# Optimization experiments

Hardware: AMD Instinct MI355X
Metric: run time of the kernel (lower is better)

## Reference

```python
import jax, jax.numpy as jnp
import numpy as np

B, L, H, P = 4, 8192, 256, 256


def discretize(log_real, imag, log_Delta, B_real, B_imag):
    # Lambda = -exp(log_real) + i*imag ; ZOH discretization
    Lr = -jnp.exp(log_real)
    Li = imag
    Delta = jnp.exp(log_Delta)
    ad = Lr * Delta
    bd = Li * Delta
    exp_ad = jnp.exp(ad)
    Lbar_r = exp_ad * jnp.cos(bd)
    Lbar_i = exp_ad * jnp.sin(bd)
    denom = jnp.maximum(Lr * Lr + Li * Li, 1e-12)
    inv_Lr = Lr / denom
    inv_Li = -Li / denom
    diff_r = Lbar_r - 1.0
    diff_i = Lbar_i
    coeff_r = inv_Lr * diff_r - inv_Li * diff_i
    coeff_i = inv_Lr * diff_i + inv_Li * diff_r
    B_bar_r = coeff_r[:, None] * B_real - coeff_i[:, None] * B_imag
    B_bar_i = coeff_r[:, None] * B_imag + coeff_i[:, None] * B_real
    return Lbar_r, Lbar_i, B_bar_r, B_bar_i


def binop(ei, ej):
    Ar_i, Ai_i, xr_i, xi_i = ei
    Ar_j, Ai_j, xr_j, xi_j = ej
    return (Ar_j * Ar_i - Ai_j * Ai_i,
            Ar_j * Ai_i + Ai_j * Ar_i,
            Ar_j * xr_i - Ai_j * xi_i + xr_j,
            Ar_j * xi_i + Ai_j * xr_i + xi_j)


def apply_ssm(Lbar_r, Lbar_i, B_bar_r, B_bar_i, C_real, C_imag, D, x):
    # x: (B,L,H), B_bar: (P,H), C: (H,P)
    Bu_r = jnp.einsum('blh,ph->blp', x, B_bar_r)
    Bu_i = jnp.einsum('blh,ph->blp', x, B_bar_i)
    A_r = jnp.broadcast_to(Lbar_r, Bu_r.shape)
    A_i = jnp.broadcast_to(Lbar_i, Bu_i.shape)
    _, _, xs_r, xs_i = jax.lax.associative_scan(binop, (A_r, A_i, Bu_r, Bu_i), axis=1)
    ys = jnp.einsum('blp,hp->blh', xs_r, C_real) - jnp.einsum('blp,hp->blh', xs_i, C_imag)
    return ys + D * x


def s5(log_real, imag, log_Delta, B_real, B_imag, C_real, C_imag, D, x):
    Lbar_r, Lbar_i, B_bar_r, B_bar_i = discretize(log_real, imag, log_Delta, B_real, B_imag)
    y = apply_ssm(Lbar_r, Lbar_i, B_bar_r, B_bar_i, C_real, C_imag, D, x)
    return jax.nn.gelu(y, approximate=False)


def setup_inputs() -> dict:
    key = jax.random.key(0)
    ks = jax.random.split(key, 17)
    std_b = 1.0 / H ** 0.5
    std_c = 1.0 / P ** 0.5
    def params(ki):
        k = jax.random.split(ks[ki], 8)
        return dict(
            log_real=jax.random.normal(k[0], (P,), jnp.float32) * 0.5,
            imag=jax.random.normal(k[1], (P,), jnp.float32),
            log_Delta=jnp.zeros((P,), jnp.float32),
            B_real=jax.random.normal(k[2], (P, H), jnp.float32) * std_b,
            B_imag=jax.random.normal(k[3], (P, H), jnp.float32) * std_b,
            C_real=jax.random.normal(k[4], (H, P), jnp.float32) * std_c,
            C_imag=jax.random.normal(k[5], (H, P), jnp.float32) * std_c,
            D=jnp.ones((H,), jnp.float32),
        )
    f = params(1)
    b = params(2)
    inp = {'x': jax.random.normal(ks[0], (B, L, H), jnp.float32)}
    for name, v in f.items():
        inp['fwd_' + name] = v
    for name, v in b.items():
        inp['bwd_' + name] = v
    return inp


def reference(x,
              fwd_log_real, fwd_imag, fwd_log_Delta, fwd_B_real, fwd_B_imag,
              fwd_C_real, fwd_C_imag, fwd_D,
              bwd_log_real, bwd_imag, bwd_log_Delta, bwd_B_real, bwd_B_imag,
              bwd_C_real, bwd_C_imag, bwd_D):
    x_flip = jnp.flip(x, axis=1)
    y_f = s5(fwd_log_real, fwd_imag, fwd_log_Delta, fwd_B_real, fwd_B_imag,
             fwd_C_real, fwd_C_imag, fwd_D, x)
    y_b = s5(bwd_log_real, bwd_imag, bwd_log_Delta, bwd_B_real, bwd_B_imag,
             bwd_C_real, bwd_C_imag, bwd_D, x_flip)
    return y_f + jnp.flip(y_b, axis=1)
```

## Files before the change

### kernel.cpp

```cpp
#include <hip/hip_runtime.h>
#include <math.h>

#define B_DIM 4
#define L_DIM 8192
#define H_DIM 256
#define P_DIM 256
#define M_DIM (B_DIM * L_DIM)
#define NC 64
#define LC 128

typedef __attribute__((ext_vector_type(8))) short bf16x8;
typedef __attribute__((ext_vector_type(4))) float f32x4;

static __device__ __forceinline__ float bf2f(unsigned int u) {
    union { unsigned int i; float f; } v; v.i = u << 16; return v.f;
}
static __device__ __forceinline__ unsigned short f2bf(float f) {
    union { float f; unsigned int i; } v; v.f = f;
    unsigned int r = v.i + 0x7FFFu + ((v.i >> 16) & 1u);
    return (unsigned short)(r >> 16);
}
static __device__ __forceinline__ float gelu_f(float x) {
    float z = 0.7978845608028654f * (x + 0.044715f * x * x * x);
    float e = __expf(2.0f * z);
    float t = 1.0f - 2.0f / (e + 1.0f);
    return 0.5f * x * (1.0f + t);
}
static __device__ __forceinline__ void async_load16(const void* g, void* l) {
    __builtin_amdgcn_global_load_lds(
        (const __attribute__((address_space(1))) unsigned int*)g,
        (__attribute__((address_space(3))) unsigned int*)l, 16, 0, 0);
}

__global__ void prep_kernel(const float* fLr, const float* fIm, const float* fLd,
                            const float* fBr, const float* fBi,
                            const float* fCr, const float* fCi,
                            const float* bLr, const float* bIm, const float* bLd,
                            const float* bBr, const float* bBi,
                            const float* bCr, const float* bCi,
                            const float4* __restrict__ x4, ushort4* __restrict__ xb,
                            unsigned short* Bmat, unsigned short* B3, float2* LbarWS) {
    int gid = blockIdx.x * 256 + threadIdx.x;
    if (gid < 2097152) {
        float4 v = x4[gid];
        ushort4 o;
        o.x = f2bf(v.x); o.y = f2bf(v.y); o.z = f2bf(v.z); o.w = f2bf(v.w);
        xb[gid] = o;
        return;
    }
    int g1 = gid - 2097152;
    if (g1 < 262144) {
        int k = g1 >> 8, h = g1 & 255;
        int d = k >> 9, pc = k & 511, p = pc >> 1, comp = pc & 1;
        const float* LR = d ? bLr : fLr;
        const float* IM = d ? bIm : fIm;
        const float* LD = d ? bLd : fLd;
        const float* BR = d ? bBr : fBr;
        const float* BI = d ? bBi : fBi;
        float Lr = -expf(LR[p]);
        float Li = IM[p];
        float Delta = expf(LD[p]);
        float ea = expf(Lr * Delta);
        float bd = Li * Delta;
        float Lbr = ea * cosf(bd);
        float Lbi = ea * sinf(bd);
        float denom = fmaxf(Lr * Lr + Li * Li, 1e-12f);
        float ivr = Lr / denom, ivi = -Li / denom;
        float dr = Lbr - 1.0f, di = Lbi;
        float cr = ivr * dr - ivi * di;
        float ci = ivr * di + ivi * dr;
        float br = BR[p * 256 + h], bi = BI[p * 256 + h];
        float val = comp ? (cr * bi + ci * br) : (cr * br - ci * bi);
        Bmat[g1] = f2bf(val);
    } else if (g1 < 524288) {
        int g2 = g1 - 262144;
        int d = g2 >> 17;
        int rem = g2 & 131071;
        int h = rem >> 9;
        int kk = rem & 511;
        int p = kk >> 1, comp = kk & 1;
        const float* CR = d ? bCr : fCr;
        const float* CI = d ? bCi : fCi;
        float val = comp ? -CI[h * 256 + p] : CR[h * 256 + p];
        B3[g2] = f2bf(val);
    } else if (g1 < 524800) {
        int g2 = g1 - 524288;
        int d = g2 >> 8, p = g2 & 255;
        const float* LR = d ? bLr : fLr;
        const float* IM = d ? bIm : fIm;
        const float* LD = d ? bLd : fLd;
        float Lr = -expf(LR[p]); float Li = IM[p]; float Delta = expf(LD[p]);
        float ea = expf(Lr * Delta); float bd = Li * Delta;
        LbarWS[g2] = make_float2(ea * cosf(bd), ea * sinf(bd));
    }
}

__global__ __launch_bounds__(256, 2) void k1_gemm(const unsigned short* __restrict__ A,
                                                  const unsigned short* __restrict__ Bm,
                                                  unsigned short* __restrict__ Bu,
                                                  const float2* __restrict__ Lbar,
                                                  float2* __restrict__ carry,
                                                  float2* __restrict__ halfc) {
    __shared__ unsigned short SH[16384];
    __shared__ float2 Sbuf[64];
    int tid = threadIdx.x;
    int lane = tid & 63, wv = tid >> 6;
    int wm = (wv >> 1) * 64, wn = (wv & 1) * 64;
    int Mb = blockIdx.x * 128, Nb = blockIdx.y * 128;
    int lr = lane >> 3;
    int swz = ((lane & 7) ^ lr) * 8;
    f32x4 acc[4][4];
#pragma unroll
    for (int i = 0; i < 4; i++)
#pragma unroll
        for (int j = 0; j < 4; j++) acc[i][j] = (f32x4){0.f, 0.f, 0.f, 0.f};
    int mrow = lane & 15, quad = lane >> 4;
    for (int kb = 0; kb < 256; kb += 64) {
#pragma unroll
        for (int ch = wv; ch < 16; ch += 4) {
            int r = ch * 8 + lr;
            async_load16(A  + (size_t)(Mb + r) * 256 + kb + swz, (char*)SH + ch * 1024);
            async_load16(Bm + (size_t)(Nb + r) * 256 + kb + swz, (char*)SH + 16384 + ch * 1024);
        }
        __syncthreads();
#pragma unroll
        for (int kk = 0; kk < 64; kk += 32) {
            bf16x8 af[4], bfr[4];
#pragma unroll
            for (int i = 0; i < 4; i++) {
                int rr = wm + 16 * i + mrow;
                af[i] = *(const bf16x8*)&SH[rr * 64 + ((((kk >> 3) + quad) ^ (rr & 7)) << 3)];
            }
#pragma unroll
            for (int j = 0; j < 4; j++) {
                int rr = wn + 16 * j + mrow;
                bfr[j] = *(const bf16x8*)&SH[8192 + rr * 64 + ((((kk >> 3) + quad) ^ (rr & 7)) << 3)];
            }
#pragma unroll
            for (int i = 0; i < 4; i++)
#pragma unroll
                for (int j = 0; j < 4; j++)
                    acc[i][j] = __builtin_amdgcn_mfma_f32_16x16x32_bf16(af[i], bfr[j], acc[i][j], 0, 0, 0);
        }
        __syncthreads();
    }
    unsigned short* Cs = SH;
#pragma unroll
    for (int i = 0; i < 4; i++)
#pragma unroll
        for (int j = 0; j < 4; j++)
#pragma unroll
            for (int r = 0; r < 4; r++) {
                int row = wm + 16 * i + quad * 4 + r;
                int col = wn + 16 * j + mrow;
                Cs[row * 128 + col] = f2bf(acc[i][j][r]);
            }
    __syncthreads();
#pragma unroll
    for (int it = 0; it < 8; it++) {
        int o = tid * 16 + it * 4096;
        int row = o >> 8, colb = o & 255;
        uint4 v = *(const uint4*)((const char*)Cs + o);
        *(uint4*)((char*)Bu + (size_t)(Mb + row) * 2048 + (size_t)Nb * 2 + colb) = v;
    }
    int d = Nb >> 9;
    int b = Mb >> 13;
    int c = (Mb >> 7) & 63;
    float sr = 0.f, si = 0.f;
    float2 A2 = make_float2(0.f, 0.f);
    int p = 0;
    if (tid < 128) {
        int j = tid & 63, half = tid >> 6;
        p = ((Nb & 511) >> 1) + j;
        A2 = Lbar[d * 256 + p];
        const unsigned int* C32 = (const unsigned int*)Cs;
        int r0 = half * 64;
        if (d == 0) {
            for (int t = 0; t < 64; t++) {
                unsigned int v = C32[(r0 + t) * 64 + j];
                float zr = bf2f(v & 0xffffu), zi = bf2f(v >> 16);
                float nr = A2.x * sr - A2.y * si + zr;
                float ni = A2.x * si + A2.y * sr + zi;
                sr = nr; si = ni;
            }
        } else {
            for (int t = 63; t >= 0; t--) {
                unsigned int v = C32[(r0 + t) * 64 + j];
                float zr = bf2f(v & 0xffffu), zi = bf2f(v >> 16);
                float nr = A2.x * sr - A2.y * si + zr;
                float ni = A2.x * si + A2.y * sr + zi;
                sr = nr; si = ni;
            }
        }
        if (half == 1) Sbuf[j] = make_float2(sr, si);
    }
    __syncthreads();
    if (tid < 64) {
        float2 S1 = Sbuf[tid];
        float a64r = A2.x, a64i = A2.y;
#pragma unroll
        for (int k = 0; k < 6; k++) {
            float nr = a64r * a64r - a64i * a64i;
            float ni = 2.f * a64r * a64i;
            a64r = nr; a64i = ni;
        }
        float cr, ci;
        float2 hv;
        if (d == 0) {
            cr = a64r * sr - a64i * si + S1.x;
            ci = a64r * si + a64i * sr + S1.y;
            hv = make_float2(sr, si);
        } else {
            cr = sr + a64r * S1.x - a64i * S1.y;
            ci = si + a64r * S1.y + a64i * S1.x;
            hv = S1;
        }
        size_t cidx = ((size_t)(d * 4 + b) * NC + c) * 256 + p;
        carry[cidx] = make_float2(cr, ci);
        halfc[cidx] = hv;
    }
}

__global__ __launch_bounds__(512) void scan_fix_kernel(unsigned int* __restrict__ XSu,
                                                       const float2* __restrict__ Lbar,
                                                       const float2* __restrict__ carry,
                                                       const float2* __restrict__ halfc) {
    int m = blockIdx.x, b = blockIdx.y;
    int c = m >> 1, h = m & 1;
    int d = threadIdx.x >> 8;
    int p = threadIdx.x & 255;
    float2 A = Lbar[d * 256 + p];
    float ar = A.x, ai = A.y;
    float a64r = ar, a64i = ai;
#pragma unroll
    for (int k = 0; k < 6; k++) {
        float nr = a64r * a64r - a64i * a64i;
        float ni = 2.f * a64r * a64i;
        a64r = nr; a64i = ni;
    }
    float a128r = a64r * a64r - a64i * a64i;
    float a128i = 2.f * a64r * a64i;
    float sr = 0.f, si = 0.f;
    const float2* cb = carry + ((size_t)(d * 4 + b) * NC) * 256 + p;
    size_t hidx = ((size_t)(d * 4 + b) * NC + c) * 256 + p;
    if (d == 0) {
#pragma unroll 4
        for (int j = 0; j < c; j++) {
            float2 cj = cb[(size_t)j * 256];
            float nr = a128r * sr - a128i * si + cj.x;
            float ni = a128r * si + a128i * sr + cj.y;
            sr = nr; si = ni;
        }
        if (h) {
            float2 hc = halfc[hidx];
            float nr = a64r * sr - a64i * si + hc.x;
            float ni = a64r * si + a64i * sr + hc.y;
            sr = nr; si = ni;
        }
    } else {
#pragma unroll 4
        for (int j = NC - 1; j > c; j--) {
            float2 cj = cb[(size_t)j * 256];
            float nr = a128r * sr - a128i * si + cj.x;
            float ni = a128r * si + a128i * sr + cj.y;
            sr = nr; si = ni;
        }
        if (!h) {
            float2 hc = halfc[hidx];
            float nr = a64r * sr - a64i * si + hc.x;
            float ni = a64r * si + a64i * sr + hc.y;
            sr = nr; si = ni;
        }
    }
    size_t base = (size_t)b * L_DIM * 512 + d * 256 + p;
    int l0 = c * 128 + h * 64;
    if (d == 0) {
#pragma unroll 16
        for (int t = 0; t < 64; t++) {
            size_t idx = base + (size_t)(l0 + t) * 512;
            unsigned int v = XSu[idx];
            float zr = bf2f(v & 0xffffu), zi = bf2f(v >> 16);
            float nr = ar * sr - ai * si + zr;
            float ni = ar * si + ai * sr + zi;
            sr = nr; si = ni;
            XSu[idx] = (unsigned int)f2bf(sr) | ((unsigned int)f2bf(si) << 16);
        }
    } else {
#pragma unroll 16
        for (int t = 63; t >= 0; t--) {
            size_t idx = base + (size_t)(l0 + t) * 512;
            unsigned int v = XSu[idx];
            float zr = bf2f(v & 0xffffu), zi = bf2f(v >> 16);
            float nr = ar * sr - ai * si + zr;
            float ni = ar * si + ai * sr + zi;
            sr = nr; si = ni;
            XSu[idx] = (unsigned int)f2bf(sr) | ((unsigned int)f2bf(si) << 16);
        }
    }
}

static __device__ __forceinline__ void k3_half(const unsigned short* __restrict__ XS,
                                               const unsigned short* __restrict__ B3h,
                                               unsigned short* As, unsigned short* Bs,
                                               int Mb, int Hb, int coff,
                                               int wm, int wn, int mrow, int quad,
                                               int lr, int swz, int wv,
                                               f32x4 (&acc)[4][4]) {
    for (int kb = 0; kb < 512; kb += 64) {
#pragma unroll
        for (int ch = wv; ch < 16; ch += 4) {
            int r = ch * 8 + lr;
            async_load16(XS + (size_t)(Mb + r) * 1024 + coff + kb + swz, (char*)As + ch * 1024);
            async_load16(B3h + (size_t)(Hb + r) * 512 + kb + swz, (char*)Bs + ch * 1024);
        }
        __syncthreads();
#pragma unroll
        for (int kk = 0; kk < 64; kk += 32) {
            bf16x8 af[4], bfr[4];
#pragma unroll
            for (int i = 0; i < 4; i++) {
                int rr = wm + 16 * i + mrow;
                af[i] = *(const bf16x8*)&As[rr * 64 + ((((kk >> 3) + quad) ^ (rr & 7)) << 3)];
            }
#pragma unroll
            for (int j = 0; j < 4; j++) {
                int rr = wn + 16 * j + mrow;
                bfr[j] = *(const bf16x8*)&Bs[rr * 64 + ((((kk >> 3) + quad) ^ (rr & 7)) << 3)];
            }
#pragma unroll
            for (int i = 0; i < 4; i++)
#pragma unroll
                for (int j = 0; j < 4; j++)
                    acc[i][j] = __builtin_amdgcn_mfma_f32_16x16x32_bf16(af[i], bfr[j], acc[i][j], 0, 0, 0);
        }
        __syncthreads();
    }
}

__global__ __launch_bounds__(256, 2) void k3_gemm(const unsigned short* __restrict__ XS,
                                                  const unsigned short* __restrict__ B3,
                                                  const unsigned short* __restrict__ xbf,
                                                  const float* __restrict__ Df,
                                                  const float* __restrict__ Db,
                                                  float* __restrict__ out) {
    __shared__ unsigned short As[128 * 64];
    __shared__ unsigned short Bs[128 * 64];
    int tid = threadIdx.x;
    int lane = tid & 63, wv = tid >> 6;
    int wm = (wv >> 1) * 64, wn = (wv & 1) * 64;
    int Mb = blockIdx.x * 128, Hb = blockIdx.y * 128;
    int lr = lane >> 3;
    int swz = ((lane & 7) ^ lr) * 8;
    int mrow = lane & 15, quad = lane >> 4;
    f32x4 accf[4][4], accb[4][4];
#pragma unroll
    for (int i = 0; i < 4; i++)
#pragma unroll
        for (int j = 0; j < 4; j++) {
            accf[i][j] = (f32x4){0.f, 0.f, 0.f, 0.f};
            accb[i][j] = (f32x4){0.f, 0.f, 0.f, 0.f};
        }
    k3_half(XS, B3,          As, Bs, Mb, Hb, 0,   wm, wn, mrow, quad, lr, swz, wv, accf);
    k3_half(XS, B3 + 131072, As, Bs, Mb, Hb, 512, wm, wn, mrow, quad, lr, swz, wv, accb);
#pragma unroll
    for (int i = 0; i < 4; i++)
#pragma unroll
        for (int j = 0; j < 4; j++) {
            int h = Hb + wn + 16 * j + mrow;
            float df = Df[h], db = Db[h];
#pragma unroll
            for (int r = 0; r < 4; r++) {
                int row = Mb + wm + 16 * i + quad * 4 + r;
                float xv = bf2f((unsigned int)xbf[(size_t)row * 256 + h]);
                float yf = accf[i][j][r] + df * xv;
                float yb = accb[i][j][r] + db * xv;
                out[(size_t)row * 256 + h] = gelu_f(yf) + gelu_f(yb);
            }
        }
}

extern "C" void kernel_launch(void* const* d_in, const int* in_sizes, int n_in,
                              void* d_out, int out_size, void* d_ws, size_t ws_size,
                              hipStream_t stream) {
    const float* x   = (const float*)d_in[0];
    const float* fLr = (const float*)d_in[1];
    const float* fIm = (const float*)d_in[2];
    const float* fLd = (const float*)d_in[3];
    const float* fBr = (const float*)d_in[4];
    const float* fBi = (const float*)d_in[5];
    const float* fCr = (const float*)d_in[6];
    const float* fCi = (const float*)d_in[7];
    const float* fD  = (const float*)d_in[8];
    const float* bLr = (const float*)d_in[9];
    const float* bIm = (const float*)d_in[10];
    const float* bLd = (const float*)d_in[11];
    const float* bBr = (const float*)d_in[12];
    const float* bBi = (const float*)d_in[13];
    const float* bCr = (const float*)d_in[14];
    const float* bCi = (const float*)d_in[15];
    const float* bD  = (const float*)d_in[16];
    float* out = (float*)d_out;

    char* ws = (char*)d_ws;
    unsigned short* xbf  = (unsigned short*)(ws);
    unsigned short* Bu   = (unsigned short*)(ws + 16777216);
    unsigned short* Bmat = (unsigned short*)(ws + 16777216 + 67108864);
    unsigned short* B3   = (unsigned short*)(ws + 16777216 + 67108864 + 524288);
    float2* LbarWS = (float2*)(ws + 16777216 + 67108864 + 1048576);
    float2* carry  = (float2*)(ws + 16777216 + 67108864 + 1048576 + 4096);
    float2* halfc  = (float2*)(ws + 16777216 + 67108864 + 1048576 + 4096 + 1048576);

    prep_kernel<<<10242, 256, 0, stream>>>(fLr, fIm, fLd, fBr, fBi, fCr, fCi,
                                           bLr, bIm, bLd, bBr, bBi, bCr, bCi,
                                           (const float4*)x, (ushort4*)xbf,
                                           Bmat, B3, LbarWS);
    k1_gemm<<<dim3(256, 8), 256, 0, stream>>>(xbf, Bmat, Bu, LbarWS, carry, halfc);
    scan_fix_kernel<<<dim3(128, 4), 512, 0, stream>>>((unsigned int*)Bu, LbarWS, carry, halfc);
    k3_gemm<<<dim3(256, 2), 256, 0, stream>>>(Bu, B3, xbf, fD, bD, out);
}
```

Before: 199.4 us.

## Fuse chunk scan fix-up into output GEMM using per-16-row carry snapshots

Removes the separate scan_fix kernel, which re-read and rewrote the whole Bu buffer. k1 now records the scan state at every 16 rows and writes 8 sub-chunk prefixes per chunk. k3 first combines the chunk carries into a prefix, then rescans each 16-row slice of the A tile in shared memory before the MFMA step. This saves a full read-modify-write pass over the 64MB intermediate. In exchange it adds serial scan work, an extra barrier per k-step and redundant carry prefix loops inside the GEMM kernel, and its UL, Ptab and LbarL arrays add about 24KB of shared memory per block.

Result: no change. 199.4 us (-0.0%).

```diff
diff --git a/kernel.cpp b/kernel.cpp
--- a/kernel.cpp
+++ b/kernel.cpp
@@ -30,6 +30,15 @@
     __builtin_amdgcn_global_load_lds(
         (const __attribute__((address_space(1))) unsigned int*)g,
         (__attribute__((address_space(3))) unsigned int*)l, 16, 0, 0);
+}
+static __device__ __forceinline__ float2 cmul2(float2 a, float2 b) {
+    return make_float2(a.x * b.x - a.y * b.y, a.x * b.y + a.y * b.x);
+}
+static __device__ __forceinline__ float2 csq2(float2 a) {
+    return make_float2(a.x * a.x - a.y * a.y, 2.f * a.x * a.y);
+}
+static __device__ __forceinline__ float2 cmad(float2 A, float2 s, float2 z) {
+    return make_float2(A.x * s.x - A.y * s.y + z.x, A.x * s.y + A.y * s.x + z.y);
 }
 
 __global__ void prep_kernel(const float* fLr, const float* fIm, const float* fLd,
@@ -100,9 +109,9 @@
                                                   unsigned short* __restrict__ Bu,
                                                   const float2* __restrict__ Lbar,
                                                   float2* __restrict__ carry,
-                                                  float2* __restrict__ halfc) {
+                                                  float2* __restrict__ Usub) {
     __shared__ unsigned short SH[16384];
-    __shared__ float2 Sbuf[64];
+    __shared__ float2 Sbuf2[64][4];
     int tid = threadIdx.x;
     int lane = tid & 63, wv = tid >> 6;
     int wm = (wv >> 1) * 64, wn = (wv & 1) * 64;
@@ -166,8 +175,10 @@
     int d = Nb >> 9;
     int b = Mb >> 13;
     int c = (Mb >> 7) & 63;
-    float sr = 0.f, si = 0.f;
+    float2 s = make_float2(0.f, 0.f);
     float2 A2 = make_float2(0.f, 0.f);
+    float2 snap[3];
+    snap[0] = snap[1] = snap[2] = make_float2(0.f, 0.f);
     int p = 0;
     if (tid < 128) {
         int j = tid & 63, half = tid >> 6;
@@ -178,134 +189,77 @@
         if (d == 0) {
             for (int t = 0; t < 64; t++) {
                 unsigned int v = C32[(r0 + t) * 64 + j];
-                float zr = bf2f(v & 0xffffu), zi = bf2f(v >> 16);
-                float nr = A2.x * sr - A2.y * si + zr;
-                float ni = A2.x * si + A2.y * sr + zi;
-                sr = nr; si = ni;
+                float2 z = make_float2(bf2f(v & 0xffffu), bf2f(v >> 16));
+                s = cmad(A2, s, z);
+                if ((t & 15) == 15 && t < 63) snap[t >> 4] = s;
             }
         } else {
             for (int t = 63; t >= 0; t--) {
                 unsigned int v = C32[(r0 + t) * 64 + j];
-                float zr = bf2f(v & 0xffffu), zi = bf2f(v >> 16);
-                float nr = A2.x * sr - A2.y * si + zr;
-                float ni = A2.x * si + A2.y * sr + zi;
-                sr = nr; si = ni;
-            }
-        }
-        if (half == 1) Sbuf[j] = make_float2(sr, si);
+                float2 z = make_float2(bf2f(v & 0xffffu), bf2f(v >> 16));
+                s = cmad(A2, s, z);
+                if ((t & 15) == 0 && t > 0) snap[(t >> 4) - 1] = s;
+            }
+        }
+        if (half == 1) {
+            Sbuf2[j][0] = snap[0]; Sbuf2[j][1] = snap[1];
+            Sbuf2[j][2] = snap[2]; Sbuf2[j][3] = s;
+        }
     }
     __syncthreads();
     if (tid < 64) {
-        float2 S1 = Sbuf[tid];
-        float a64r = A2.x, a64i = A2.y;
-#pragma unroll
-        for (int k = 0; k < 6; k++) {
-            float nr = a64r * a64r - a64i * a64i;
-            float ni = 2.f * a64r * a64i;
-            a64r = nr; a64i = ni;
-        }
-        float cr, ci;
-        float2 hv;
+        float2 h1a = Sbuf2[tid][0], h1b = Sbuf2[tid][1], h1c = Sbuf2[tid][2], S1 = Sbuf2[tid][3];
+        float2 a16 = A2;
+#pragma unroll
+        for (int k = 0; k < 4; k++) a16 = csq2(a16);
+        float2 a32 = csq2(a16);
+        float2 a48 = cmul2(a32, a16);
+        float2 a64 = csq2(a32);
+        float2 S0 = s;
+        float2 Uq[8];
+        float2 cfull;
+        float2 zero = make_float2(0.f, 0.f);
         if (d == 0) {
-            cr = a64r * sr - a64i * si + S1.x;
-            ci = a64r * si + a64i * sr + S1.y;
-            hv = make_float2(sr, si);
+            Uq[0] = zero;  Uq[1] = snap[0]; Uq[2] = snap[1]; Uq[3] = snap[2];
+            Uq[4] = S0;
+            Uq[5] = cmad(a16, S0, h1a);
+            Uq[6] = cmad(a32, S0, h1b);
+            Uq[7] = cmad(a48, S0, h1c);
+            cfull = cmad(a64, S0, S1);
         } else {
-            cr = sr + a64r * S1.x - a64i * S1.y;
-            ci = si + a64r * S1.y + a64i * S1.x;
-            hv = S1;
+            Uq[7] = zero;
+            Uq[6] = h1c;
+            Uq[5] = h1b;
+            Uq[4] = h1a;
+            Uq[3] = S1;
+            Uq[2] = cmad(a16, S1, snap[2]);
+            Uq[1] = cmad(a32, S1, snap[1]);
+            Uq[0] = cmad(a48, S1, snap[0]);
+            cfull = cmad(a64, S1, S0);
         }
         size_t cidx = ((size_t)(d * 4 + b) * NC + c) * 256 + p;
-        carry[cidx] = make_float2(cr, ci);
-        halfc[cidx] = hv;
-    }
-}
-
-__global__ __launch_bounds__(512) void scan_fix_kernel(unsigned int* __restrict__ XSu,
-                                                       const float2* __restrict__ Lbar,
-                                                       const float2* __restrict__ carry,
-                                                       const float2* __restrict__ halfc) {
-    int m = blockIdx.x, b = blockIdx.y;
-    int c = m >> 1, h = m & 1;
-    int d = threadIdx.x >> 8;
-    int p = threadIdx.x & 255;
-    float2 A = Lbar[d * 256 + p];
-    float ar = A.x, ai = A.y;
-    float a64r = ar, a64i = ai;
-#pragma unroll
-    for (int k = 0; k < 6; k++) {
-        float nr = a64r * a64r - a64i * a64i;
-        float ni = 2.f * a64r * a64i;
-        a64r = nr; a64i = ni;
-    }
-    float a128r = a64r * a64r - a64i * a64i;
-    float a128i = 2.f * a64r * a64i;
-    float sr = 0.f, si = 0.f;
-    const float2* cb = carry + ((size_t)(d * 4 + b) * NC) * 256 + p;
-    size_t hidx = ((size_t)(d * 4 + b) * NC + c) * 256 + p;
-    if (d == 0) {
-#pragma unroll 4
-        for (int j = 0; j < c; j++) {
-            float2 cj = cb[(size_t)j * 256];
-            float nr = a128r * sr - a128i * si + cj.x;
-            float ni = a128r * si + a128i * sr + cj.y;
-            sr = nr; si = ni;
-        }
-        if (h) {
-            float2 hc = halfc[hidx];
-            float nr = a64r * sr - a64i * si + hc.x;
-            float ni = a64r * si + a64i * sr + hc.y;
-            sr = nr; si = ni;
-        }
-    } else {
-#pragma unroll 4
-        for (int j = NC - 1; j > c; j--) {
-            float2 cj = cb[(size_t)j * 256];
-            float nr = a128r * sr - a128i * si + cj.x;
-            float ni = a128r * si + a128i * sr + cj.y;
-            sr = nr; si = ni;
-        }
-        if (!h) {
-            float2 hc = halfc[hidx];
-            float nr = a64r * sr - a64i * si + hc.x;
-            float ni = a64r * si + a64i * sr + hc.y;
-            sr = nr; si = ni;
-        }
-    }
-    size_t base = (size_t)b * L_DIM * 512 + d * 256 + p;
-    int l0 = c * 128 + h * 64;
-    if (d == 0) {
-#pragma unroll 16
-        for (int t = 0; t < 64; t++) {
-            size_t idx = base + (size_t)(l0 + t) * 512;
-            unsigned int v = XSu[idx];
-            float zr = bf2f(v & 0xffffu), zi = bf2f(v >> 16);
-            float nr = ar * sr - ai * si + zr;
-            float ni = ar * si + ai * sr + zi;
-            sr = nr; si = ni;
-            XSu[idx] = (unsigned int)f2bf(sr) | ((unsigned int)f2bf(si) << 16);
-        }
-    } else {
-#pragma unroll 16
-        for (int t = 63; t >= 0; t--) {
-            size_t idx = base + (size_t)(l0 + t) * 512;
-            unsigned int v = XSu[idx];
-            float zr = bf2f(v & 0xffffu), zi = bf2f(v >> 16);
-            float nr = ar * sr - ai * si + zr;
-            float ni = ar * si + ai * sr + zi;
-            sr = nr; si = ni;
-            XSu[idx] = (unsigned int)f2bf(sr) | ((unsigned int)f2bf(si) << 16);
-        }
+        carry[cidx] = cfull;
+        size_t ub = (((size_t)(d * 4 + b) * NC + c) * 8) * 256 + p;
+#pragma unroll
+        for (int q = 0; q < 8; q++) Usub[ub + (size_t)q * 256] = Uq[q];
     }
 }
 
 static __device__ __forceinline__ void k3_half(const unsigned short* __restrict__ XS,
                                                const unsigned short* __restrict__ B3h,
                                                unsigned short* As, unsigned short* Bs,
-                                               int Mb, int Hb, int coff,
+                                               float2* UL, const float2* Ptab, const float2* LbarL,
+                                               const float2* __restrict__ Uchunk,
+                                               int Mb, int Hb, int coff, int d,
                                                int wm, int wn, int mrow, int quad,
-                                               int lr, int swz, int wv,
+                                               int lr, int swz, int wv, int tid,
                                                f32x4 (&acc)[4][4]) {
+#pragma unroll
+    for (int it = 0; it < 4; it++)
+        async_load16((const char*)Uchunk + (size_t)(wv * 4 + it) * 1024 + (size_t)(tid & 63) * 16,
+                     (char*)UL + (wv * 4 + it) * 1024);
+    int j = tid & 31, q = tid >> 5;
+    int r0 = q * 16;
     for (int kb = 0; kb < 512; kb += 64) {
 #pragma unroll
         for (int ch = wv; ch < 16; ch += 4) {
@@ -314,6 +268,51 @@
             async_load16(B3h + (size_t)(Hb + r) * 512 + kb + swz, (char*)Bs + ch * 1024);
         }
         __syncthreads();
+        {
+            int p = (kb >> 1) + j;
+            float2 Ac = LbarL[d * 256 + p];
+            float2 P  = Ptab[d * 256 + p];
+            float2 U  = UL[q * 256 + p];
+            int e = d ? (7 - q) : q;
+            float2 ap = make_float2(1.f, 0.f);
+            float2 bp = Ac;
+#pragma unroll
+            for (int k = 0; k < 4; k++) bp = csq2(bp);
+            if (e & 1) ap = cmul2(ap, bp);
+            bp = csq2(bp);
+            if (e & 2) ap = cmul2(ap, bp);
+            bp = csq2(bp);
+            if (e & 4) ap = cmul2(ap, bp);
+            float2 s = cmad(ap, P, U);
+            unsigned int* A32 = (unsigned int*)As;
+            unsigned int zb[16];
+#pragma unroll
+            for (int t = 0; t < 16; t++) {
+                int row = r0 + t;
+                zb[t] = A32[row * 32 + (((j >> 2) ^ (row & 7)) << 2) + (j & 3)];
+            }
+            if (d == 0) {
+#pragma unroll
+                for (int t = 0; t < 16; t++) {
+                    float2 z = make_float2(bf2f(zb[t] & 0xffffu), bf2f(zb[t] >> 16));
+                    s = cmad(Ac, s, z);
+                    zb[t] = (unsigned int)f2bf(s.x) | ((unsigned int)f2bf(s.y) << 16);
+                }
+            } else {
+#pragma unroll
+                for (int t = 15; t >= 0; t--) {
+                    float2 z = make_float2(bf2f(zb[t] & 0xffffu), bf2f(zb[t] >> 16));
+                    s = cmad(Ac, s, z);
+                    zb[t] = (unsigned int)f2bf(s.x) | ((unsigned int)f2bf(s.y) << 16);
+                }
+            }
+#pragma unroll
+            for (int t = 0; t < 16; t++) {
+                int row = r0 + t;
+                A32[row * 32 + (((j >> 2) ^ (row & 7)) << 2) + (j & 3)] = zb[t];
+            }
+        }
+        __syncthreads();
 #pragma unroll
         for (int kk = 0; kk < 64; kk += 32) {
             bf16x8 af[4], bfr[4];
@@ -323,15 +322,15 @@
                 af[i] = *(const bf16x8*)&As[rr * 64 + ((((kk >> 3) + quad) ^ (rr & 7)) << 3)];
             }
 #pragma unroll
-            for (int j = 0; j < 4; j++) {
-                int rr = wn + 16 * j + mrow;
-                bfr[j] = *(const bf16x8*)&Bs[rr * 64 + ((((kk >> 3) + quad) ^ (rr & 7)) << 3)];
+            for (int jj2 = 0; jj2 < 4; jj2++) {
+                int rr = wn + 16 * jj2 + mrow;
+                bfr[jj2] = *(const bf16x8*)&Bs[rr * 64 + ((((kk >> 3) + quad) ^ (rr & 7)) << 3)];
             }
 #pragma unroll
             for (int i = 0; i < 4; i++)
 #pragma unroll
-                for (int j = 0; j < 4; j++)
-                    acc[i][j] = __builtin_amdgcn_mfma_f32_16x16x32_bf16(af[i], bfr[j], acc[i][j], 0, 0, 0);
+                for (int jj2 = 0; jj2 < 4; jj2++)
+                    acc[i][jj2] = __builtin_amdgcn_mfma_f32_16x16x32_bf16(af[i], bfr[jj2], acc[i][jj2], 0, 0, 0);
         }
         __syncthreads();
     }
@@ -342,16 +341,45 @@
                                                   const unsigned short* __restrict__ xbf,
                                                   const float* __restrict__ Df,
                                                   const float* __restrict__ Db,
+                                                  const float2* __restrict__ Lbar,
+                                                  const float2* __restrict__ carry,
+                                                  const float2* __restrict__ Usub,
                                                   float* __restrict__ out) {
     __shared__ unsigned short As[128 * 64];
     __shared__ unsigned short Bs[128 * 64];
+    __shared__ float2 UL[2048];
+    __shared__ float2 Ptab[512];
+    __shared__ float2 LbarL[512];
     int tid = threadIdx.x;
     int lane = tid & 63, wv = tid >> 6;
     int wm = (wv >> 1) * 64, wn = (wv & 1) * 64;
     int Mb = blockIdx.x * 128, Hb = blockIdx.y * 128;
+    int b = Mb >> 13, c = (Mb >> 7) & 63;
     int lr = lane >> 3;
     int swz = ((lane & 7) ^ lr) * 8;
     int mrow = lane & 15, quad = lane >> 4;
+    {
+        int p0 = tid;
+#pragma unroll
+        for (int d2 = 0; d2 < 2; d2++) {
+            float2 A = Lbar[d2 * 256 + p0];
+            LbarL[d2 * 256 + p0] = A;
+            float2 a128 = A;
+#pragma unroll
+            for (int k = 0; k < 7; k++) a128 = csq2(a128);
+            float2 s = make_float2(0.f, 0.f);
+            const float2* cb = carry + ((size_t)(d2 * 4 + b) * NC) * 256 + p0;
+            if (d2 == 0) {
+#pragma unroll 16
+                for (int jj = 0; jj < c; jj++) s = cmad(a128, s, cb[(size_t)jj * 256]);
+            } else {
+#pragma unroll 16
+                for (int jj = NC - 1; jj > c; jj--) s = cmad(a128, s, cb[(size_t)jj * 256]);
+            }
+            Ptab[d2 * 256 + p0] = s;
+        }
+    }
+    __syncthreads();
     f32x4 accf[4][4], accb[4][4];
 #pragma unroll
     for (int i = 0; i < 4; i++)
@@ -360,8 +388,12 @@
             accf[i][j] = (f32x4){0.f, 0.f, 0.f, 0.f};
             accb[i][j] = (f32x4){0.f, 0.f, 0.f, 0.f};
         }
-    k3_half(XS, B3,          As, Bs, Mb, Hb, 0,   wm, wn, mrow, quad, lr, swz, wv, accf);
-    k3_half(XS, B3 + 131072, As, Bs, Mb, Hb, 512, wm, wn, mrow, quad, lr, swz, wv, accb);
+    const float2* U0 = Usub + (((size_t)(0 * 4 + b) * NC + c) * 8) * 256;
+    const float2* U1 = Usub + (((size_t)(1 * 4 + b) * NC + c) * 8) * 256;
+    k3_half(XS, B3,          As, Bs, UL, Ptab, LbarL, U0, Mb, Hb, 0,   0,
+            wm, wn, mrow, quad, lr, swz, wv, tid, accf);
+    k3_half(XS, B3 + 131072, As, Bs, UL, Ptab, LbarL, U1, Mb, Hb, 512, 1,
+            wm, wn, mrow, quad, lr, swz, wv, tid, accb);
 #pragma unroll
     for (int i = 0; i < 4; i++)
 #pragma unroll
@@ -408,13 +440,12 @@
     unsigned short* B3   = (unsigned short*)(ws + 16777216 + 67108864 + 524288);
     float2* LbarWS = (float2*)(ws + 16777216 + 67108864 + 1048576);
     float2* carry  = (float2*)(ws + 16777216 + 67108864 + 1048576 + 4096);
-    float2* halfc  = (float2*)(ws + 16777216 + 67108864 + 1048576 + 4096 + 1048576);
+    float2* Usub   = (float2*)(ws + 16777216 + 67108864 + 1048576 + 4096 + 1048576);
 
     prep_kernel<<<10242, 256, 0, stream>>>(fLr, fIm, fLd, fBr, fBi, fCr, fCi,
                                            bLr, bIm, bLd, bBr, bBi, bCr, bCi,
                                            (const float4*)x, (ushort4*)xbf,
                                            Bmat, B3, LbarWS);
-    k1_gemm<<<dim3(256, 8), 256, 0, stream>>>(xbf, Bmat, Bu, LbarWS, carry, halfc);
-    scan_fix_kernel<<<dim3(128, 4), 512, 0, stream>>>((unsigned int*)Bu, LbarWS, carry, halfc);
-    k3_gemm<<<dim3(256, 2), 256, 0, stream>>>(Bu, B3, xbf, fD, bD, out);
-}
+    k1_gemm<<<dim3(256, 8), 256, 0, stream>>>(xbf, Bmat, Bu, LbarWS, carry, Usub);
+    k3_gemm<<<dim3(256, 2), 256, 0, stream>>>(Bu, B3, xbf, fD, bD, LbarWS, carry, Usub, out);
+}
```
